# Kernel optimization log

Hardware: AMD Instinct MI355X
Metric: run time of the kernel (lower is better)

Reference implementation:

```python
import jax, jax.numpy as jnp
import numpy as np

N_NODES = 100000

def setup_inputs() -> dict:
    key = jax.random.key(0)
    k1, k2, k3, k4, k5 = jax.random.split(key, 5)
    F_in, H, C = 128, 64, 40
    x = jax.random.normal(k1, (N_NODES, F_in), dtype=jnp.float32)
    edge_index = jax.random.randint(k2, (2, 1600000), 0, N_NODES, dtype=jnp.int64)
    # GCNConv weights (no bias), Glorot-ish scale
    W0 = jax.random.normal(k3, (F_in, H), dtype=jnp.float32) / np.sqrt(F_in)
    W1 = jax.random.normal(k4, (H, H), dtype=jnp.float32) / np.sqrt(H)
    W2 = jax.random.normal(k5, (H, C), dtype=jnp.float32) / np.sqrt(H)
    return {"x": x, "edge_index": edge_index, "W0": W0, "W1": W1, "W2": W2}


def _gcn_norm(edge_index, num_nodes):
    # Add self-loops, compute symmetric normalization D^-1/2 A D^-1/2
    loop = jnp.arange(num_nodes, dtype=edge_index.dtype)
    src = jnp.concatenate([edge_index[0], loop])
    dst = jnp.concatenate([edge_index[1], loop])
    deg = jax.ops.segment_sum(jnp.ones_like(dst, dtype=jnp.float32), dst,
                              num_segments=num_nodes)
    dinv = jnp.where(deg > 0, jax.lax.rsqrt(deg), 0.0)
    norm = dinv[src] * dinv[dst]  # [E + N]
    return src, dst, norm


def reference(x, edge_index, W0, W1, W2):
    N = x.shape[0]
    src, dst, norm = _gcn_norm(edge_index, N)

    def conv(h, W):
        h = h @ W                                   # [N, d_out]
        msg = h[src] * norm[:, None]                # gather + scale  [E+N, d_out]
        return jax.ops.segment_sum(msg, dst, num_segments=N)

    h = jax.nn.relu(conv(x, W0))
    h = jax.nn.relu(conv(h, W1))
    h = jax.nn.relu(conv(h, W2))
    return h
```

## Files before the change

kernel.cpp:

```cpp
#include <hip/hip_runtime.h>
#include <hip/hip_fp16.h>

#define N_FEAT0 128
#define HID 64
#define NCLS 40

#define BSH 9
#define BSZ 512
#define BCAP 12288
#define STILE 4096

typedef _Float16 half8 __attribute__((ext_vector_type(8)));
typedef float f32x4 __attribute__((ext_vector_type(4)));

__global__ __launch_bounds__(256) void scatter_kernel(const int* __restrict__ esrc,
                                                      const int* __restrict__ edst,
                                                      int* __restrict__ bfill,
                                                      int* __restrict__ slab, int E) {
  __shared__ int cnt[256];
  __shared__ int base[256];
  int t = threadIdx.x;
  int t0 = blockIdx.x * STILE;
  cnt[t] = 0;
  __syncthreads();

#pragma unroll 4
  for (int i = 0; i < STILE / 1024; ++i) {
    int e = t0 + i * 1024 + t * 4;
    if (e < E) {
      int4 d4 = *(const int4*)(edst + e);
      atomicAdd(&cnt[d4.x >> BSH], 1);
      atomicAdd(&cnt[d4.y >> BSH], 1);
      atomicAdd(&cnt[d4.z >> BSH], 1);
      atomicAdd(&cnt[d4.w >> BSH], 1);
    }
  }
  __syncthreads();
  int c = cnt[t];
  if (c > 0) base[t] = t * BCAP + atomicAdd(&bfill[t], c);
  cnt[t] = 0;
  __syncthreads();

#pragma unroll 4
  for (int i = 0; i < STILE / 1024; ++i) {
    int e = t0 + i * 1024 + t * 4;
    if (e < E) {
      int4 s4 = *(const int4*)(esrc + e);
      int4 d4 = *(const int4*)(edst + e);
#define EMIT(dd, ss)                                             \
      {                                                          \
        int b_ = (dd) >> BSH;                                    \
        int r_ = atomicAdd(&cnt[b_], 1);                         \
        slab[base[b_] + r_] = (((dd) & (BSZ - 1)) << 17) | (ss); \
      }
      EMIT(d4.x, s4.x)
      EMIT(d4.y, s4.y)
      EMIT(d4.z, s4.z)
      EMIT(d4.w, s4.w)
#undef EMIT
    }
  }
}

__global__ __launch_bounds__(512) void build_kernel(const int* __restrict__ slab,
                                                    const int* __restrict__ bfill,
                                                    int* __restrict__ row_ptr,
                                                    float* __restrict__ dinv,
                                                    int* __restrict__ ew,
                                                    int N, int nbuck) {
  __shared__ int cnt[512];
  __shared__ int pre[512];
  __shared__ int sc[256];
  int b = blockIdx.x;
  int t = threadIdx.x;
  int nbase = b << BSH;
  int nNodes = N - nbase;
  if (nNodes > BSZ) nNodes = BSZ;

  if (t < 256) sc[t] = (t < nbuck) ? bfill[t] : 0;
  __syncthreads();
  for (int off = 1; off < 256; off <<= 1) {
    int u = 0;
    if (t < 256 && t >= off) u = sc[t - off];
    __syncthreads();
    if (t < 256) sc[t] += u;
    __syncthreads();
  }
  int sz = bfill[b];
  int obase = sc[b] - sz;
  if (b == 0 && t == 0) row_ptr[N] = sc[255];
  cnt[t] = 0;
  __syncthreads();

  int sbeg = b * BCAP;

  for (int r = t; r < sz; r += 512) atomicAdd(&cnt[((unsigned)slab[sbeg + r]) >> 17], 1);
  __syncthreads();

  int c = cnt[t];
  pre[t] = c;
  __syncthreads();
  for (int off = 1; off < 512; off <<= 1) {
    int u = (t >= off) ? pre[t - off] : 0;
    __syncthreads();
    pre[t] += u;
    __syncthreads();
  }
  int ex = pre[t] - c;

  if (t < nNodes) {
    row_ptr[nbase + t] = obase + ex;
    dinv[nbase + t] = rsqrtf((float)(c + 1));
  }
  __syncthreads();
  pre[t] = ex;
  cnt[t] = 0;
  __syncthreads();

  for (int r = t; r < sz; r += 512) {
    int rec = slab[sbeg + r];
    int dloc = ((unsigned)rec) >> 17;
    int rank = atomicAdd(&cnt[dloc], 1);
    ew[obase + pre[dloc] + rank] = rec & 0x1FFFF;
  }
}

__global__ __launch_bounds__(256) void prep_w_kernel(const float* __restrict__ W0,
                                                     const float* __restrict__ W1,
                                                     const float* __restrict__ W2,
                                                     __half* __restrict__ Wt0,
                                                     __half* __restrict__ Wt1,
                                                     __half* __restrict__ Wt2) {
  int id = blockIdx.x * 256 + threadIdx.x;
  if (id < 8192) {
    int c = id >> 7, k = id & 127;
    Wt0[id] = __float2half_rn(W0[k * 64 + c]);
  } else if (id < 8192 + 4096) {
    int i = id - 8192;
    int c = i >> 6, k = i & 63;
    Wt1[i] = __float2half_rn(W1[k * 64 + c]);
  } else if (id < 8192 + 4096 + 3072) {
    int i = id - 8192 - 4096;
    int c = i >> 6, k = i & 63;
    Wt2[i] = (c < NCLS) ? __float2half_rn(W2[k * NCLS + c]) : __half(0.f);
  }
}

template <int K, int NC, bool AF32>
__global__ __launch_bounds__(256) void gemm_mfma(const void* __restrict__ Av,
                                                 const __half* __restrict__ Wt,
                                                 __half* __restrict__ Out,
                                                 const float* __restrict__ dinv,
                                                 int N) {
  constexpr int NT = (NC + 15) / 16;
  int lane = threadIdx.x & 63;
  int r16 = lane & 15;
  int kq = lane >> 4;
  int wid = blockIdx.x * 4 + (threadIdx.x >> 6);
  int ntiles = (N + 15) >> 4;
  if (wid >= ntiles) return;
  int r0 = wid << 4;

  const __half* Ah = (const __half*)Av;
  const float* Af = (const float*)Av;
  int arow = r0 + r16;
  if (arow >= N) arow = N - 1;

  f32x4 acc[NT];
#pragma unroll
  for (int t2 = 0; t2 < NT; ++t2) acc[t2] = (f32x4){0.f, 0.f, 0.f, 0.f};

#pragma unroll
  for (int s = 0; s < K / 32; ++s) {
    half8 a;
    if constexpr (AF32) {
      const float* ap = Af + (size_t)arow * K + s * 32 + kq * 8;
      float4 v0 = *(const float4*)ap;
      float4 v1 = *(const float4*)(ap + 4);
      a[0] = (_Float16)v0.x; a[1] = (_Float16)v0.y;
      a[2] = (_Float16)v0.z; a[3] = (_Float16)v0.w;
      a[4] = (_Float16)v1.x; a[5] = (_Float16)v1.y;
      a[6] = (_Float16)v1.z; a[7] = (_Float16)v1.w;
    } else {
      a = *(const half8*)(Ah + (size_t)arow * K + s * 32 + kq * 8);
    }
#pragma unroll
    for (int t2 = 0; t2 < NT; ++t2) {
      half8 b = *(const half8*)(Wt + (size_t)(t2 * 16 + r16) * K + s * 32 + kq * 8);
      acc[t2] = __builtin_amdgcn_mfma_f32_16x16x32_f16(a, b, acc[t2], 0, 0, 0);
    }
  }

  float4 dv = *(const float4*)(dinv + r0 + kq * 4);
  float ds[4] = {dv.x, dv.y, dv.z, dv.w};
#pragma unroll
  for (int b = 0; b < 4; ++b) {
    int gr = r0 + kq * 4 + b;
#pragma unroll
    for (int t2 = 0; t2 < NT; ++t2) {
      int col = t2 * 16 + r16;
      if (col < NC) Out[(size_t)gr * NC + col] = __float2half_rn(ds[b] * acc[t2][b]);
    }
  }
}

template <int F, bool HOUT>
__global__ __launch_bounds__(256) void agg_kernel(const __half* __restrict__ G,
                                                  const int* __restrict__ row_ptr,
                                                  const int* __restrict__ ew,
                                                  const float* __restrict__ dinv,
                                                  void* __restrict__ HoutV, int N) {
  constexpr int FO = F / 8;
  int gid = blockIdx.x * blockDim.x + threadIdx.x;
  int v = gid >> 6;
  if (v >= N) return;
  int lane = threadIdx.x & 63;
  int eg = lane >> 3;
  int fo = lane & 7;
  bool fok = (fo < FO);
  int foc = fok ? fo : FO - 1;

  float acc[8];
#pragma unroll
  for (int i = 0; i < 8; ++i) acc[i] = 0.f;

#define GLD(s) (*(const uint4*)(G + (size_t)(s) * F + foc * 8))
  auto addrow = [&](uint4 q) {
    const __half2* h = (const __half2*)&q;
#pragma unroll
    for (int i = 0; i < 4; ++i) {
      float2 f = __half22float2(h[i]);
      acc[2 * i] += f.x;
      acc[2 * i + 1] += f.y;
    }
  };

  if (eg == 0) addrow(GLD(v));

  int beg = __builtin_amdgcn_readfirstlane(row_ptr[v]);
  int end = __builtin_amdgcn_readfirstlane(row_ptr[v + 1]);
  int j = beg;
  for (; j + 16 <= end; j += 16) {
    int s0 = ew[j + eg];
    int s1 = ew[j + 8 + eg];
    uint4 a = GLD(s0);
    uint4 b = GLD(s1);
    addrow(a);
    addrow(b);
  }
  if (j + 8 <= end) {
    addrow(GLD(ew[j + eg]));
    j += 8;
  }
  {
    int idx = j + eg;
    if (idx < end) addrow(GLD(ew[idx]));
  }
#undef GLD

#pragma unroll
  for (int m = 8; m <= 32; m <<= 1) {
#pragma unroll
    for (int i = 0; i < 8; ++i) acc[i] += __shfl_xor(acc[i], m);
  }

  if (fok) {
    float dv = dinv[v];
    if constexpr (HOUT) {
      __half* Hout = (__half*)HoutV;
      union { __half2 h2[4]; uint4 u; } cv;
      cv.h2[0] = __floats2half2_rn(fmaxf(dv * acc[0], 0.f), fmaxf(dv * acc[1], 0.f));
      cv.h2[1] = __floats2half2_rn(fmaxf(dv * acc[2], 0.f), fmaxf(dv * acc[3], 0.f));
      cv.h2[2] = __floats2half2_rn(fmaxf(dv * acc[4], 0.f), fmaxf(dv * acc[5], 0.f));
      cv.h2[3] = __floats2half2_rn(fmaxf(dv * acc[6], 0.f), fmaxf(dv * acc[7], 0.f));
      *(uint4*)(Hout + (size_t)v * F + fo * 8) = cv.u;
    } else {
      float* Hout = (float*)HoutV;
      float4 o0, o1;
      o0.x = fmaxf(dv * acc[0], 0.f);
      o0.y = fmaxf(dv * acc[1], 0.f);
      o0.z = fmaxf(dv * acc[2], 0.f);
      o0.w = fmaxf(dv * acc[3], 0.f);
      o1.x = fmaxf(dv * acc[4], 0.f);
      o1.y = fmaxf(dv * acc[5], 0.f);
      o1.z = fmaxf(dv * acc[6], 0.f);
      o1.w = fmaxf(dv * acc[7], 0.f);
      float4* outp = (float4*)(Hout + (size_t)v * F + fo * 8);
      outp[0] = o0;
      outp[1] = o1;
    }
  }
}

extern "C" void kernel_launch(void* const* d_in, const int* in_sizes, int n_in,
                              void* d_out, int out_size, void* d_ws, size_t ws_size,
                              hipStream_t stream) {
  const float* x  = (const float*)d_in[0];
  const int*   eg = (const int*)d_in[1];
  const float* W0 = (const float*)d_in[2];
  const float* W1 = (const float*)d_in[3];
  const float* W2 = (const float*)d_in[4];
  float* out = (float*)d_out;

  const int N = in_sizes[0] / N_FEAT0;
  const int E = in_sizes[1] / 2;
  const int* esrc = eg;
  const int* edst = eg + E;
  const int nbuck = (N + BSZ - 1) >> BSH;

  char* p = (char*)d_ws;
  auto alloc = [&](size_t bytes) {
    char* r = p;
    p += (bytes + 255) & ~(size_t)255;
    return r;
  };
  int*    bfill   = (int*)alloc(256 * 4);
  int*    row_ptr = (int*)alloc((size_t)(N + 1) * 4);
  float*  dinv    = (float*)alloc((size_t)N * 4);
  int*    ew      = (int*)alloc((size_t)E * 4);
  __half* Wt0     = (__half*)alloc(8192 * 2);
  __half* Wt1     = (__half*)alloc(4096 * 2);
  __half* Wt2     = (__half*)alloc(3072 * 2);
  __half* bufG    = (__half*)alloc((size_t)N * HID * 2);
  __half* bufH    = (__half*)alloc((size_t)N * HID * 2);
  __half* bufG3   = (__half*)alloc((size_t)N * NCLS * 2);
  int* slab = (int*)bufH;

  hipMemsetAsync(bfill, 0, 256 * 4, stream);

  prep_w_kernel<<<60, 256, 0, stream>>>(W0, W1, W2, Wt0, Wt1, Wt2);
  const int sblocks = (E + STILE - 1) / STILE;
  scatter_kernel<<<sblocks, 256, 0, stream>>>(esrc, edst, bfill, slab, E);
  build_kernel<<<nbuck, 512, 0, stream>>>(slab, bfill, row_ptr, dinv, ew, N, nbuck);

  const int ntiles = (N + 15) / 16;
  const int mblocks = (ntiles + 3) / 4;
  const int ablocks = (N + 3) / 4;
  gemm_mfma<128, 64, true><<<mblocks, 256, 0, stream>>>(x, Wt0, bufG, dinv, N);
  agg_kernel<64, true><<<ablocks, 256, 0, stream>>>(bufG, row_ptr, ew, dinv, bufH, N);
  gemm_mfma<64, 64, false><<<mblocks, 256, 0, stream>>>(bufH, Wt1, bufG, dinv, N);
  agg_kernel<64, true><<<ablocks, 256, 0, stream>>>(bufG, row_ptr, ew, dinv, bufH, N);
  gemm_mfma<64, 40, false><<<mblocks, 256, 0, stream>>>(bufH, Wt2, bufG3, dinv, N);
  agg_kernel<40, false><<<ablocks, 256, 0, stream>>>(bufG3, row_ptr, ew, dinv, out, N);
}
```

Before: 303.8 us.

## Split CSR build into hist/scan/perm kernels with 4x block parallelism

The single build kernel, which ran one block per 512-node bucket (about 196 blocks), is split into three kernels. A histogram kernel uses four blocks per bucket and global atomics into a per-node counts array. A scan kernel computes row_ptr and dinv. A permute kernel uses four blocks per bucket and places edges with global atomicSub on the counts. The scatter kernel now also keeps src/dst in registers from the first pass instead of reloading them. This raises parallelism on the slab passes at the cost of two extra launches, global atomics, and a larger memset.

```diff
diff --git a/kernel.cpp b/kernel.cpp
--- a/kernel.cpp
+++ b/kernel.cpp
@@ -24,15 +24,19 @@
   cnt[t] = 0;
   __syncthreads();
 
-#pragma unroll 4
-  for (int i = 0; i < STILE / 1024; ++i) {
+  int4 s4[4], d4[4];
+  bool ok[4];
+#pragma unroll
+  for (int i = 0; i < 4; ++i) {
     int e = t0 + i * 1024 + t * 4;
-    if (e < E) {
-      int4 d4 = *(const int4*)(edst + e);
-      atomicAdd(&cnt[d4.x >> BSH], 1);
-      atomicAdd(&cnt[d4.y >> BSH], 1);
-      atomicAdd(&cnt[d4.z >> BSH], 1);
-      atomicAdd(&cnt[d4.w >> BSH], 1);
+    ok[i] = (e < E);
+    if (ok[i]) {
+      s4[i] = *(const int4*)(esrc + e);
+      d4[i] = *(const int4*)(edst + e);
+      atomicAdd(&cnt[d4[i].x >> BSH], 1);
+      atomicAdd(&cnt[d4[i].y >> BSH], 1);
+      atomicAdd(&cnt[d4[i].z >> BSH], 1);
+      atomicAdd(&cnt[d4[i].w >> BSH], 1);
     }
   }
   __syncthreads();
@@ -41,42 +45,56 @@
   cnt[t] = 0;
   __syncthreads();
 
-#pragma unroll 4
-  for (int i = 0; i < STILE / 1024; ++i) {
-    int e = t0 + i * 1024 + t * 4;
-    if (e < E) {
-      int4 s4 = *(const int4*)(esrc + e);
-      int4 d4 = *(const int4*)(edst + e);
+#pragma unroll
+  for (int i = 0; i < 4; ++i) {
+    if (ok[i]) {
 #define EMIT(dd, ss)                                             \
       {                                                          \
         int b_ = (dd) >> BSH;                                    \
         int r_ = atomicAdd(&cnt[b_], 1);                         \
         slab[base[b_] + r_] = (((dd) & (BSZ - 1)) << 17) | (ss); \
       }
-      EMIT(d4.x, s4.x)
-      EMIT(d4.y, s4.y)
-      EMIT(d4.z, s4.z)
-      EMIT(d4.w, s4.w)
+      EMIT(d4[i].x, s4[i].x)
+      EMIT(d4[i].y, s4[i].y)
+      EMIT(d4[i].z, s4[i].z)
+      EMIT(d4[i].w, s4[i].w)
 #undef EMIT
     }
   }
 }
 
-__global__ __launch_bounds__(512) void build_kernel(const int* __restrict__ slab,
-                                                    const int* __restrict__ bfill,
-                                                    int* __restrict__ row_ptr,
-                                                    float* __restrict__ dinv,
-                                                    int* __restrict__ ew,
-                                                    int N, int nbuck) {
-  __shared__ int cnt[512];
+__global__ __launch_bounds__(256) void hist_kernel(const int* __restrict__ slab,
+                                                   const int* __restrict__ bfill,
+                                                   int* __restrict__ counts, int N) {
+  __shared__ int h[512];
+  int b = blockIdx.x >> 2;
+  int q = blockIdx.x & 3;
+  int t = threadIdx.x;
+  h[t] = 0;
+  h[t + 256] = 0;
+  __syncthreads();
+  int sz = bfill[b];
+  int sbeg = b * BCAP;
+  int r0 = (int)(((long long)sz * q) >> 2);
+  int r1 = (int)(((long long)sz * (q + 1)) >> 2);
+  for (int r = r0 + t; r < r1; r += 256)
+    atomicAdd(&h[((unsigned)slab[sbeg + r]) >> 17], 1);
+  __syncthreads();
+  int nbase = b << BSH;
+  if (nbase + t < N && h[t]) atomicAdd(&counts[nbase + t], h[t]);
+  int t2 = t + 256;
+  if (nbase + t2 < N && h[t2]) atomicAdd(&counts[nbase + t2], h[t2]);
+}
+
+__global__ __launch_bounds__(512) void scan_kernel(const int* __restrict__ bfill,
+                                                   const int* __restrict__ counts,
+                                                   int* __restrict__ row_ptr,
+                                                   float* __restrict__ dinv,
+                                                   int N, int nbuck) {
+  __shared__ int sc[256];
   __shared__ int pre[512];
-  __shared__ int sc[256];
   int b = blockIdx.x;
   int t = threadIdx.x;
-  int nbase = b << BSH;
-  int nNodes = N - nbase;
-  if (nNodes > BSZ) nNodes = BSZ;
-
   if (t < 256) sc[t] = (t < nbuck) ? bfill[t] : 0;
   __syncthreads();
   for (int off = 1; off < 256; off <<= 1) {
@@ -86,18 +104,12 @@
     if (t < 256) sc[t] += u;
     __syncthreads();
   }
-  int sz = bfill[b];
-  int obase = sc[b] - sz;
+  int obase = sc[b] - bfill[b];
   if (b == 0 && t == 0) row_ptr[N] = sc[255];
-  cnt[t] = 0;
-  __syncthreads();
-
-  int sbeg = b * BCAP;
-
-  for (int r = t; r < sz; r += 512) atomicAdd(&cnt[((unsigned)slab[sbeg + r]) >> 17], 1);
-  __syncthreads();
-
-  int c = cnt[t];
+  int nbase = b << BSH;
+  int nNodes = N - nbase;
+  if (nNodes > BSZ) nNodes = BSZ;
+  int c = (t < nNodes) ? counts[nbase + t] : 0;
   pre[t] = c;
   __syncthreads();
   for (int off = 1; off < 512; off <<= 1) {
@@ -106,22 +118,37 @@
     pre[t] += u;
     __syncthreads();
   }
-  int ex = pre[t] - c;
-
   if (t < nNodes) {
-    row_ptr[nbase + t] = obase + ex;
+    row_ptr[nbase + t] = obase + pre[t] - c;
     dinv[nbase + t] = rsqrtf((float)(c + 1));
   }
-  __syncthreads();
-  pre[t] = ex;
-  cnt[t] = 0;
-  __syncthreads();
-
-  for (int r = t; r < sz; r += 512) {
+}
+
+__global__ __launch_bounds__(256) void perm_kernel(const int* __restrict__ slab,
+                                                   const int* __restrict__ bfill,
+                                                   const int* __restrict__ row_ptr,
+                                                   int* __restrict__ counts,
+                                                   int* __restrict__ ew, int N) {
+  __shared__ int rp[512];
+  int b = blockIdx.x >> 2;
+  int q = blockIdx.x & 3;
+  int t = threadIdx.x;
+  int nbase = b << BSH;
+  int nNodes = N - nbase;
+  if (nNodes > BSZ) nNodes = BSZ;
+  if (t < nNodes) rp[t] = row_ptr[nbase + t];
+  int t2 = t + 256;
+  if (t2 < nNodes) rp[t2] = row_ptr[nbase + t2];
+  __syncthreads();
+  int sz = bfill[b];
+  int sbeg = b * BCAP;
+  int r0 = (int)(((long long)sz * q) >> 2);
+  int r1 = (int)(((long long)sz * (q + 1)) >> 2);
+  for (int r = r0 + t; r < r1; r += 256) {
     int rec = slab[sbeg + r];
     int dloc = ((unsigned)rec) >> 17;
-    int rank = atomicAdd(&cnt[dloc], 1);
-    ew[obase + pre[dloc] + rank] = rec & 0x1FFFF;
+    int rank = atomicSub(&counts[nbase + dloc], 1) - 1;
+    ew[rp[dloc] + rank] = rec & 0x1FFFF;
   }
 }
 
@@ -315,6 +342,7 @@
     return r;
   };
   int*    bfill   = (int*)alloc(256 * 4);
+  int*    counts  = (int*)alloc((size_t)N * 4);
   int*    row_ptr = (int*)alloc((size_t)(N + 1) * 4);
   float*  dinv    = (float*)alloc((size_t)N * 4);
   int*    ew      = (int*)alloc((size_t)E * 4);
@@ -326,12 +354,15 @@
   __half* bufG3   = (__half*)alloc((size_t)N * NCLS * 2);
   int* slab = (int*)bufH;
 
-  hipMemsetAsync(bfill, 0, 256 * 4, stream);
+  hipMemsetAsync(bfill, 0, (size_t)((char*)counts - (char*)bfill) + (size_t)N * 4,
+                 stream);
 
   prep_w_kernel<<<60, 256, 0, stream>>>(W0, W1, W2, Wt0, Wt1, Wt2);
   const int sblocks = (E + STILE - 1) / STILE;
   scatter_kernel<<<sblocks, 256, 0, stream>>>(esrc, edst, bfill, slab, E);
-  build_kernel<<<nbuck, 512, 0, stream>>>(slab, bfill, row_ptr, dinv, ew, N, nbuck);
+  hist_kernel<<<nbuck * 4, 256, 0, stream>>>(slab, bfill, counts, N);
+  scan_kernel<<<nbuck, 512, 0, stream>>>(bfill, counts, row_ptr, dinv, N, nbuck);
+  perm_kernel<<<nbuck * 4, 256, 0, stream>>>(slab, bfill, row_ptr, counts, ew, N);
 
   const int ntiles = (N + 15) / 16;
   const int mblocks = (ntiles + 3) / 4;
```

After: 346.8 us. 14.1% more time.
